# Optimization experiments

Hardware: AMD Instinct MI355X
Metric: run time of the kernel (lower is better)

Reference implementation:

```python
import jax, jax.numpy as jnp
import numpy as np

N, F, H = 512, 256, 512

def _w(k, i, o):
    return jax.random.normal(k, (i, o), jnp.float32) * (1.0 / np.sqrt(i))

def setup_inputs() -> dict:
    key = jax.random.key(0)
    ks = jax.random.split(key, 12)
    z = lambda n: jnp.zeros((n,), jnp.float32)
    return {
        "node_features": jax.random.normal(ks[0], (N, F), jnp.float32),
        "adjacency": jax.random.uniform(ks[1], (N, N), jnp.float32),
        # GraphConv layers: neighbor linear (wl,bl) and self-loop (ws,bs)
        "gc1_wl": _w(ks[2], F, H), "gc1_bl": z(H), "gc1_ws": _w(ks[3], F, H), "gc1_bs": z(H),
        "gc2_wl": _w(ks[4], H, H), "gc2_bl": z(H), "gc2_ws": _w(ks[5], H, H), "gc2_bs": z(H),
        "gc3_wl": _w(ks[6], H, F), "gc3_bl": z(F), "gc3_ws": _w(ks[7], H, F), "gc3_bs": z(F),
        # edge MLP: Linear(2F,H) -> ReLU -> (dropout=identity, eval) -> Linear(H,H) -> ReLU -> Linear(H,1)
        "mlp_w1": _w(ks[8], 2 * F, H), "mlp_b1": z(H),
        "mlp_w2": _w(ks[9], H, H), "mlp_b2": z(H),
        "mlp_w3": _w(ks[10], H, 1), "mlp_b3": z(1),
    }

def _gconv(x, adj_norm, wl, bl, ws, bs):
    # adj_norm @ Linear(x) + SelfLoop(x)
    return adj_norm @ (x @ wl + bl) + (x @ ws + bs)

def reference(node_features, adjacency,
              gc1_wl, gc1_bl, gc1_ws, gc1_bs,
              gc2_wl, gc2_bl, gc2_ws, gc2_bs,
              gc3_wl, gc3_bl, gc3_ws, gc3_bs,
              mlp_w1, mlp_b1, mlp_w2, mlp_b2, mlp_w3, mlp_b3):
    # row-normalized adjacency (shared across all three layers)
    adj_norm = adjacency / (adjacency.sum(axis=1, keepdims=True) + 1e-8)
    x = jax.nn.relu(_gconv(node_features, adj_norm, gc1_wl, gc1_bl, gc1_ws, gc1_bs))
    x = jax.nn.relu(_gconv(x, adj_norm, gc2_wl, gc2_bl, gc2_ws, gc2_bs))
    emb = _gconv(x, adj_norm, gc3_wl, gc3_bl, gc3_ws, gc3_bs)  # [N, F]
    # vectorized all-pairs (i<j) edge scoring, symmetric scatter
    iu, ju = np.triu_indices(N, k=1)  # static index lists, P = N(N-1)/2
    ef = jnp.concatenate([emb[iu], emb[ju]], axis=-1)  # [P, 2F]
    h = jax.nn.relu(ef @ mlp_w1 + mlp_b1)
    h = jax.nn.relu(h @ mlp_w2 + mlp_b2)
    s = jax.nn.sigmoid((h @ mlp_w3 + mlp_b3)[:, 0])  # [P]
    edge_scores = jnp.zeros((N, N), emb.dtype).at[iu, ju].set(s).at[ju, iu].set(s)
    return emb, edge_scores
```

## Files before the change

### kernel.cpp

```cpp
#include <hip/hip_runtime.h>
#include <hip/hip_bf16.h>


#define NN 512
#define FF 256
#define HH 512

typedef __attribute__((ext_vector_type(8))) short s8v;
typedef __attribute__((ext_vector_type(4))) float f4v;

__device__ __forceinline__ ushort f2bf(float f) {
  unsigned u = __float_as_uint(f);
  unsigned r = (u + 0x7fffu + ((u >> 16) & 1u)) >> 16;
  return (ushort)r;
}

__global__ __launch_bounds__(256)
void prep_kernel(const float* __restrict__ adj, float* __restrict__ adjn,
                 const float* __restrict__ w2, ushort* __restrict__ w2t2) {
  int b = blockIdx.x;
  int tid = threadIdx.x;
  if (b < 512) {
    const float* r = adj + b * NN;
    float a0 = r[tid], a1 = r[tid + 256];
    float s = a0 + a1;
#pragma unroll
    for (int m = 1; m < 64; m <<= 1) s += __shfl_xor(s, m);
    __shared__ float wsum[4];
    if ((tid & 63) == 0) wsum[tid >> 6] = s;
    __syncthreads();
    float inv = 1.f / (wsum[0] + wsum[1] + wsum[2] + wsum[3] + 1e-8f);
    float* o = adjn + b * NN;
    o[tid] = a0 * inv;
    o[tid + 256] = a1 * inv;
  } else {
    int b2 = b - 512;
    int slab = b2 >> 3;
    int col = (b2 & 7) * 64 + (tid >> 2);
    int kq = tid & 3;
    int k0 = slab * 32 + kq * 8;
    ushort tmp[8];
#pragma unroll
    for (int e = 0; e < 8; ++e) tmp[e] = f2bf(w2[(k0 + e) * HH + col]);
    ushort* dst = w2t2 + slab * 16384 + col * 32 + kq * 8;
    *(ushort4*)dst = *(ushort4*)tmp;
    *(ushort4*)(dst + 4) = *(ushort4*)&tmp[4];
  }
}

template <bool RELU>
__global__ __launch_bounds__(256)
void gemm_ts(int M, int N, int K,
             const float* __restrict__ A, int lda,
             const float* __restrict__ B0, const float* __restrict__ B1, int ldb,
             const float* __restrict__ bias0, const float* __restrict__ bias1,
             const float* __restrict__ add0, const float* __restrict__ add1, int ldadd,
             float* __restrict__ C0, float* __restrict__ C1, int ldc)
{
  const float* B = blockIdx.z ? B1 : B0;
  const float* bias = blockIdx.z ? bias1 : bias0;
  const float* add = blockIdx.z ? add1 : add0;
  float* C = blockIdx.z ? C1 : C0;
  const int n0 = blockIdx.x * 64;
  const int m0 = blockIdx.y * 16;
  const int tid = threadIdx.x;
  const int ty = tid >> 4, tx = tid & 15;

  __shared__ float As[32][18];
  __shared__ float Bs[32][68];
  float4 acc = {0.f, 0.f, 0.f, 0.f};

  const int am = tid >> 4;
  const int ak = tid & 15;
  const int bk = tid >> 4;
  const int bn = tid & 15;

  float2 pa = *(const float2*)&A[(m0 + am) * lda + ak * 2];
  float4 pb0 = *(const float4*)&B[bk * ldb + n0 + bn * 4];
  float4 pb1 = *(const float4*)&B[(bk + 16) * ldb + n0 + bn * 4];

  for (int k0 = 0; k0 < K; k0 += 32) {
    As[ak * 2][am] = pa.x;
    As[ak * 2 + 1][am] = pa.y;
    *(float4*)&Bs[bk][bn * 4] = pb0;
    *(float4*)&Bs[bk + 16][bn * 4] = pb1;
    __syncthreads();
    if (k0 + 32 < K) {
      pa = *(const float2*)&A[(m0 + am) * lda + k0 + 32 + ak * 2];
      pb0 = *(const float4*)&B[(k0 + 32 + bk) * ldb + n0 + bn * 4];
      pb1 = *(const float4*)&B[(k0 + 48 + bk) * ldb + n0 + bn * 4];
    }
#pragma unroll
    for (int k = 0; k < 32; ++k) {
      float a = As[k][ty];
      float4 b = *(const float4*)&Bs[k][tx * 4];
      acc.x += a * b.x; acc.y += a * b.y; acc.z += a * b.z; acc.w += a * b.w;
    }
    __syncthreads();
  }

  int m = m0 + ty;
  float4 v = acc;
  if (bias) {
    float4 bv = *(const float4*)&bias[n0 + tx * 4];
    v.x += bv.x; v.y += bv.y; v.z += bv.z; v.w += bv.w;
  }
  if (add) {
    float4 d = *(const float4*)&add[m * ldadd + n0 + tx * 4];
    v.x += d.x; v.y += d.y; v.z += d.z; v.w += d.w;
  }
  if (RELU) {
    v.x = fmaxf(v.x, 0.f); v.y = fmaxf(v.y, 0.f);
    v.z = fmaxf(v.z, 0.f); v.w = fmaxf(v.w, 0.f);
  }
  *(float4*)&C[m * ldc + n0 + tx * 4] = v;
}

__global__ __launch_bounds__(512)
__attribute__((amdgpu_waves_per_eu(2, 2)))
void edge_mlp(const float* __restrict__ Amat, const float* __restrict__ Bmat,
              const ushort* __restrict__ w2t2,
              const float* __restrict__ b2, const float* __restrict__ w3,
              const float* __restrict__ b3,
              float* __restrict__ edges)
{
  __shared__ ushort h1s[2][128 * 128];
  __shared__ float rowsv[2][24][128];
  __shared__ float part[8][128];

  const int tb = (int)blockIdx.x;
  int bj = (int)((sqrtf(4.f * tb + 1.f) - 1.f) * 0.5f);
  while (bj * bj + bj > tb) --bj;
  while ((bj + 1) * (bj + 2) <= tb) ++bj;
  const int bi = tb - bj * bj - bj;

  const int tid = threadIdx.x;
  const int wid = tid >> 6;
  const int lane = tid & 63;
  const int l15 = lane & 15;
  const int lg = lane >> 4;

  const f4v zero = {0.f, 0.f, 0.f, 0.f};
  f4v acc[8][4];
#pragma unroll
  for (int mf = 0; mf < 8; ++mf)
#pragma unroll
    for (int nf = 0; nf < 4; ++nf) acc[mf][nf] = zero;

  const int r1 = tid >> 5, kc1 = tid & 31;
  const int r2 = 16 + (tid >> 5);
  const float* src1base = (r1 < 8) ? (Amat + (bi * 8 + r1) * HH)
                                   : (Bmat + (bj * 16 + r1 - 8) * HH);
  const float* src2base = Bmat + (bj * 16 + r2 - 8) * HH;

  float4 ra, rb;
  auto issue_rows = [&](int ch) {
    ra = *(const float4*)(src1base + ch * 128 + kc1 * 4);
    if (tid < 256) rb = *(const float4*)(src2base + ch * 128 + kc1 * 4);
  };
  auto write_rows = [&](int buf) {
    *(float4*)&rowsv[buf][r1][kc1 * 4] = ra;
    if (tid < 256) *(float4*)&rowsv[buf][r2][kc1 * 4] = rb;
  };
  auto build_h1 = [&](int buf) {
#pragma unroll
    for (int q = 0; q < 8; ++q) {
      int fidx = q * 512 + tid;
      int p = fidx >> 5;
      int k4 = fidx & 31;
      float4 av = *(const float4*)&rowsv[buf][p >> 4][k4 * 4];
      float4 bv = *(const float4*)&rowsv[buf][8 + (p & 15)][k4 * 4];
      ushort4 pk;
      pk.x = f2bf(fmaxf(av.x + bv.x, 0.f));
      pk.y = f2bf(fmaxf(av.y + bv.y, 0.f));
      pk.z = f2bf(fmaxf(av.z + bv.z, 0.f));
      pk.w = f2bf(fmaxf(av.w + bv.w, 0.f));
      int off = (p * 256 + k4 * 8) ^ ((p & 7) << 4);
      *(ushort4*)((char*)h1s[buf] + off) = pk;
    }
  };

  auto lgkm_barrier = [] {
    asm volatile("s_waitcnt lgkmcnt(0)" ::: "memory");
    __builtin_amdgcn_s_barrier();
  };

  issue_rows(0);
  write_rows(0);
  lgkm_barrier();
  build_h1(0);
  lgkm_barrier();

  const ushort* wbase = w2t2 + wid * 2048 + l15 * 32 + lg * 8;

  s8v nb0, nb1, nb2, nb3;
  nb0 = *(const s8v*)wbase;
  nb1 = *(const s8v*)(wbase + 512);
  nb2 = *(const s8v*)(wbase + 1024);
  nb3 = *(const s8v*)(wbase + 1536);

  auto slab_step = [&](int cur, int slab) {
    s8v cb0 = nb0, cb1 = nb1, cb2 = nb2, cb3 = nb3;
    if (slab < 15) {
      const ushort* wb = wbase + (slab + 1) * 16384;
      nb0 = *(const s8v*)wb;
      nb1 = *(const s8v*)(wb + 512);
      nb2 = *(const s8v*)(wb + 1024);
      nb3 = *(const s8v*)(wb + 1536);
    }
    int ks = slab & 3;
    __builtin_amdgcn_s_setprio(1);
#pragma unroll
    for (int mf = 0; mf < 8; ++mf) {
      int p = mf * 16 + l15;
      int off = (p * 256 + ks * 64 + lg * 16) ^ ((p & 7) << 4);
      s8v a = *(const s8v*)((const char*)h1s[cur] + off);
      acc[mf][0] = __builtin_amdgcn_mfma_f32_16x16x32_bf16(a, cb0, acc[mf][0], 0, 0, 0);
      acc[mf][1] = __builtin_amdgcn_mfma_f32_16x16x32_bf16(a, cb1, acc[mf][1], 0, 0, 0);
      acc[mf][2] = __builtin_amdgcn_mfma_f32_16x16x32_bf16(a, cb2, acc[mf][2], 0, 0, 0);
      acc[mf][3] = __builtin_amdgcn_mfma_f32_16x16x32_bf16(a, cb3, acc[mf][3], 0, 0, 0);
    }
    __builtin_amdgcn_s_setprio(0);
  };

#pragma unroll
  for (int ch = 0; ch < 4; ++ch) {
    int cur = ch & 1;
    if (ch < 3) issue_rows(ch + 1);
    slab_step(cur, ch * 4 + 0);
    slab_step(cur, ch * 4 + 1);
    if (ch < 3) write_rows(cur ^ 1);
    slab_step(cur, ch * 4 + 2);
    if (ch < 3) lgkm_barrier();
    slab_step(cur, ch * 4 + 3);
    if (ch < 3) {
      build_h1(cur ^ 1);
      lgkm_barrier();
    }
  }

  float bb[4], ww[4];
#pragma unroll
  for (int nf = 0; nf < 4; ++nf) {
    int col = wid * 64 + nf * 16 + l15;
    bb[nf] = b2[col];
    ww[nf] = w3[col];
  }
#pragma unroll
  for (int mf = 0; mf < 8; ++mf) {
    float ps[4];
#pragma unroll
    for (int e = 0; e < 4; ++e) {
      ps[e] = fmaxf(acc[mf][0][e] + bb[0], 0.f) * ww[0] +
              fmaxf(acc[mf][1][e] + bb[1], 0.f) * ww[1] +
              fmaxf(acc[mf][2][e] + bb[2], 0.f) * ww[2] +
              fmaxf(acc[mf][3][e] + bb[3], 0.f) * ww[3];
    }
#pragma unroll
    for (int m = 1; m < 16; m <<= 1) {
#pragma unroll
      for (int e = 0; e < 4; ++e) ps[e] += __shfl_xor(ps[e], m);
    }
    if (l15 == 0) {
#pragma unroll
      for (int e = 0; e < 4; ++e)
        part[wid][mf * 16 + lg * 4 + e] = ps[e];
    }
  }
  __syncthreads();
  if (tid < 128) {
    float tot = b3[0];
#pragma unroll
    for (int w = 0; w < 8; ++w) tot += part[w][tid];
    float sg = 1.f / (1.f + expf(-tot));
    int i = bi * 8 + (tid >> 4);
    int j = bj * 16 + (tid & 15);
    if (i < j) {
      edges[i * NN + j] = sg;
      edges[j * NN + i] = sg;
    } else if (i == j) {
      edges[i * NN + i] = 0.f;
    }
  }
}

extern "C" void kernel_launch(void* const* d_in, const int* in_sizes, int n_in,
                              void* d_out, int out_size, void* d_ws, size_t ws_size,
                              hipStream_t stream) {
  const float* node = (const float*)d_in[0];
  const float* adj  = (const float*)d_in[1];
  const float* g1wl = (const float*)d_in[2];
  const float* g1bl = (const float*)d_in[3];
  const float* g1ws = (const float*)d_in[4];
  const float* g1bs = (const float*)d_in[5];
  const float* g2wl = (const float*)d_in[6];
  const float* g2bl = (const float*)d_in[7];
  const float* g2ws = (const float*)d_in[8];
  const float* g2bs = (const float*)d_in[9];
  const float* g3wl = (const float*)d_in[10];
  const float* g3bl = (const float*)d_in[11];
  const float* g3ws = (const float*)d_in[12];
  const float* g3bs = (const float*)d_in[13];
  const float* w1 = (const float*)d_in[14];
  const float* b1 = (const float*)d_in[15];
  const float* w2 = (const float*)d_in[16];
  const float* b2 = (const float*)d_in[17];
  const float* w3 = (const float*)d_in[18];
  const float* b3 = (const float*)d_in[19];

  float* out = (float*)d_out;
  float* emb = out;
  float* edges = out + NN * FF;

  char* wsb = (char*)d_ws;
  float* adjn = (float*)wsb;
  float* Tb   = (float*)(wsb + (1u << 20));
  float* Sb   = (float*)(wsb + (2u << 20));
  float* xa   = (float*)(wsb + (3u << 20));
  float* xb   = (float*)(wsb + (4u << 20));
  ushort* w2t2 = (ushort*)(wsb + (5u << 20));
  float* Amat = Tb;
  float* Bmat = Sb;

  prep_kernel<<<640, 256, 0, stream>>>(adj, adjn, w2, w2t2);

  gemm_ts<false><<<dim3(8, 32, 2), 256, 0, stream>>>(
      NN, HH, FF, node, FF, g1wl, g1ws, HH, g1bl, g1bs,
      nullptr, nullptr, 0, Tb, Sb, HH);
  gemm_ts<true><<<dim3(8, 32, 1), 256, 0, stream>>>(
      NN, HH, NN, adjn, NN, Tb, Tb, HH, nullptr, nullptr,
      Sb, Sb, HH, xa, xa, HH);
  gemm_ts<false><<<dim3(8, 32, 2), 256, 0, stream>>>(
      NN, HH, HH, xa, HH, g2wl, g2ws, HH, g2bl, g2bs,
      nullptr, nullptr, 0, Tb, Sb, HH);
  gemm_ts<true><<<dim3(8, 32, 1), 256, 0, stream>>>(
      NN, HH, NN, adjn, NN, Tb, Tb, HH, nullptr, nullptr,
      Sb, Sb, HH, xb, xb, HH);
  gemm_ts<false><<<dim3(4, 32, 2), 256, 0, stream>>>(
      NN, FF, HH, xb, HH, g3wl, g3ws, FF, g3bl, g3bs,
      nullptr, nullptr, 0, Tb, Sb, FF);
  gemm_ts<false><<<dim3(4, 32, 1), 256, 0, stream>>>(
      NN, FF, NN, adjn, NN, Tb, Tb, FF, nullptr, nullptr,
      Sb, Sb, FF, emb, emb, FF);

  gemm_ts<false><<<dim3(8, 32, 2), 256, 0, stream>>>(
      NN, HH, FF, emb, FF, w1, w1 + FF * HH, HH, b1, nullptr,
      nullptr, nullptr, 0, Amat, Bmat, HH);

  edge_mlp<<<1056, 512, 0, stream>>>(Amat, Bmat, w2t2, b2, w3, b3, edges);
}
```

Before: 188.2 us.

## Double edge_mlp block to 1024 threads with 16 waves splitting output columns

The edge MLP block grows from 8 to 16 waves. Each wave now owns 32 output columns instead of 64, which halves its accumulators and per-slab weight loads. The cooperative row loads and the h1 build are redistributed across the larger block, and the partial-sum reduction grows to 16 entries. The intent is more latency hiding per block and lower register pressure, at the cost of more waves contending for the same LDS A-fragments and more barrier participants.

```diff
diff --git a/kernel.cpp b/kernel.cpp
--- a/kernel.cpp
+++ b/kernel.cpp
@@ -116,8 +116,7 @@
   *(float4*)&C[m * ldc + n0 + tx * 4] = v;
 }
 
-__global__ __launch_bounds__(512)
-__attribute__((amdgpu_waves_per_eu(2, 2)))
+__global__ __launch_bounds__(1024)
 void edge_mlp(const float* __restrict__ Amat, const float* __restrict__ Bmat,
               const ushort* __restrict__ w2t2,
               const float* __restrict__ b2, const float* __restrict__ w3,
@@ -126,7 +125,7 @@
 {
   __shared__ ushort h1s[2][128 * 128];
   __shared__ float rowsv[2][24][128];
-  __shared__ float part[8][128];
+  __shared__ float part[16][128];
 
   const int tb = (int)blockIdx.x;
   int bj = (int)((sqrtf(4.f * tb + 1.f) - 1.f) * 0.5f);
@@ -141,31 +140,29 @@
   const int lg = lane >> 4;
 
   const f4v zero = {0.f, 0.f, 0.f, 0.f};
-  f4v acc[8][4];
-#pragma unroll
-  for (int mf = 0; mf < 8; ++mf)
-#pragma unroll
-    for (int nf = 0; nf < 4; ++nf) acc[mf][nf] = zero;
-
-  const int r1 = tid >> 5, kc1 = tid & 31;
-  const int r2 = 16 + (tid >> 5);
-  const float* src1base = (r1 < 8) ? (Amat + (bi * 8 + r1) * HH)
-                                   : (Bmat + (bj * 16 + r1 - 8) * HH);
-  const float* src2base = Bmat + (bj * 16 + r2 - 8) * HH;
-
-  float4 ra, rb;
+  f4v acc[8][2];
+#pragma unroll
+  for (int mf = 0; mf < 8; ++mf) {
+    acc[mf][0] = zero;
+    acc[mf][1] = zero;
+  }
+
+  const int rr = tid >> 5;
+  const int kc = tid & 31;
+  const bool rowAct = rr < 24;
+  const float* srcbase = (rr < 8) ? (Amat + (bi * 8 + rr) * HH)
+                                  : (Bmat + (bj * 16 + (rr - 8)) * HH);
+  float4 ra;
   auto issue_rows = [&](int ch) {
-    ra = *(const float4*)(src1base + ch * 128 + kc1 * 4);
-    if (tid < 256) rb = *(const float4*)(src2base + ch * 128 + kc1 * 4);
+    if (rowAct) ra = *(const float4*)(srcbase + ch * 128 + kc * 4);
   };
   auto write_rows = [&](int buf) {
-    *(float4*)&rowsv[buf][r1][kc1 * 4] = ra;
-    if (tid < 256) *(float4*)&rowsv[buf][r2][kc1 * 4] = rb;
+    if (rowAct) *(float4*)&rowsv[buf][rr][kc * 4] = ra;
   };
   auto build_h1 = [&](int buf) {
 #pragma unroll
-    for (int q = 0; q < 8; ++q) {
-      int fidx = q * 512 + tid;
+    for (int q = 0; q < 4; ++q) {
+      int fidx = q * 1024 + tid;
       int p = fidx >> 5;
       int k4 = fidx & 31;
       float4 av = *(const float4*)&rowsv[buf][p >> 4][k4 * 4];
@@ -191,22 +188,18 @@
   build_h1(0);
   lgkm_barrier();
 
-  const ushort* wbase = w2t2 + wid * 2048 + l15 * 32 + lg * 8;
-
-  s8v nb0, nb1, nb2, nb3;
+  const ushort* wbase = w2t2 + (wid * 32 + l15) * 32 + lg * 8;
+
+  s8v nb0, nb1;
   nb0 = *(const s8v*)wbase;
   nb1 = *(const s8v*)(wbase + 512);
-  nb2 = *(const s8v*)(wbase + 1024);
-  nb3 = *(const s8v*)(wbase + 1536);
 
   auto slab_step = [&](int cur, int slab) {
-    s8v cb0 = nb0, cb1 = nb1, cb2 = nb2, cb3 = nb3;
+    s8v cb0 = nb0, cb1 = nb1;
     if (slab < 15) {
       const ushort* wb = wbase + (slab + 1) * 16384;
       nb0 = *(const s8v*)wb;
       nb1 = *(const s8v*)(wb + 512);
-      nb2 = *(const s8v*)(wb + 1024);
-      nb3 = *(const s8v*)(wb + 1536);
     }
     int ks = slab & 3;
     __builtin_amdgcn_s_setprio(1);
@@ -217,8 +210,6 @@
       s8v a = *(const s8v*)((const char*)h1s[cur] + off);
       acc[mf][0] = __builtin_amdgcn_mfma_f32_16x16x32_bf16(a, cb0, acc[mf][0], 0, 0, 0);
       acc[mf][1] = __builtin_amdgcn_mfma_f32_16x16x32_bf16(a, cb1, acc[mf][1], 0, 0, 0);
-      acc[mf][2] = __builtin_amdgcn_mfma_f32_16x16x32_bf16(a, cb2, acc[mf][2], 0, 0, 0);
-      acc[mf][3] = __builtin_amdgcn_mfma_f32_16x16x32_bf16(a, cb3, acc[mf][3], 0, 0, 0);
     }
     __builtin_amdgcn_s_setprio(0);
   };
@@ -239,22 +230,15 @@
     }
   }
 
-  float bb[4], ww[4];
-#pragma unroll
-  for (int nf = 0; nf < 4; ++nf) {
-    int col = wid * 64 + nf * 16 + l15;
-    bb[nf] = b2[col];
-    ww[nf] = w3[col];
-  }
+  float bb0 = b2[wid * 32 + l15], bb1 = b2[wid * 32 + 16 + l15];
+  float ww0 = w3[wid * 32 + l15], ww1 = w3[wid * 32 + 16 + l15];
 #pragma unroll
   for (int mf = 0; mf < 8; ++mf) {
     float ps[4];
 #pragma unroll
     for (int e = 0; e < 4; ++e) {
-      ps[e] = fmaxf(acc[mf][0][e] + bb[0], 0.f) * ww[0] +
-              fmaxf(acc[mf][1][e] + bb[1], 0.f) * ww[1] +
-              fmaxf(acc[mf][2][e] + bb[2], 0.f) * ww[2] +
-              fmaxf(acc[mf][3][e] + bb[3], 0.f) * ww[3];
+      ps[e] = fmaxf(acc[mf][0][e] + bb0, 0.f) * ww0 +
+              fmaxf(acc[mf][1][e] + bb1, 0.f) * ww1;
     }
 #pragma unroll
     for (int m = 1; m < 16; m <<= 1) {
@@ -271,7 +255,7 @@
   if (tid < 128) {
     float tot = b3[0];
 #pragma unroll
-    for (int w = 0; w < 8; ++w) tot += part[w][tid];
+    for (int w = 0; w < 16; ++w) tot += part[w][tid];
     float sg = 1.f / (1.f + expf(-tot));
     int i = bi * 8 + (tid >> 4);
     int j = bj * 16 + (tid & 15);
@@ -347,5 +331,5 @@
       NN, HH, FF, emb, FF, w1, w1 + FF * HH, HH, b1, nullptr,
       nullptr, nullptr, 0, Amat, Bmat, HH);
 
-  edge_mlp<<<1056, 512, 0, stream>>>(Amat, Bmat, w2t2, b2, w3, b3, edges);
-}
+  edge_mlp<<<1056, 1024, 0, stream>>>(Amat, Bmat, w2t2, b2, w3, b3, edges);
+}
```

Result: slower. 215.0 us (+14.2%).
